# Optimization experiments

Hardware: AMD Instinct MI355X
Metric: run time of the kernel (lower is better)

## Reference

```python
import jax, jax.numpy as jnp
import numpy as np

D_MODEL = 512
NUM_HEADS = 8
D_HEAD = 64
B, T = 8, 1024


def sinusoidal_pos(start, end, d, dtype=jnp.float32):
    # positions start .. end-1, standard sinusoidal encoding, shape (1, end-start, d)
    pos = jnp.arange(start, end, dtype=jnp.float32)[:, None]              # (L,1)
    inv_freq = jnp.exp(-jnp.log(10000.0) * jnp.arange(0, d, 2, dtype=jnp.float32) / d)
    ang = pos * inv_freq[None, :]                                          # (L,d/2)
    pe = jnp.stack([jnp.sin(ang), jnp.cos(ang)], axis=-1).reshape(pos.shape[0], d)
    return pe[None].astype(dtype)                                          # (1,L,d)


def _relative_shift(x):
    # x: (B,H,T,L) -> Transformer-XL shift trick
    b, h, t, l = x.shape
    x = jnp.pad(x, ((0, 0), (0, 0), (0, 0), (1, 0)))                       # (B,H,T,L+1)
    x = x.reshape(b, h, l + 1, t)[:, :, 1:, :].reshape(b, h, t, l)
    return x


def setup_inputs() -> dict:
    key = jax.random.key(0)
    ks = jax.random.split(key, 8)
    hd = NUM_HEADS * D_HEAD
    s_in = 1.0 / np.sqrt(D_MODEL)
    s_out = 1.0 / np.sqrt(hd)
    return {
        "xs": jax.random.normal(ks[0], (B, T, D_MODEL), jnp.float32),
        "mask": jnp.ones((B, T, T), jnp.int32),
        "Wq": jax.random.normal(ks[1], (D_MODEL, hd), jnp.float32) * s_in,
        "Wk": jax.random.normal(ks[2], (D_MODEL, hd), jnp.float32) * s_in,
        "Wv": jax.random.normal(ks[3], (D_MODEL, hd), jnp.float32) * s_in,
        "Wpos": jax.random.normal(ks[4], (D_MODEL, hd), jnp.float32) * s_in,
        "Wout": jax.random.normal(ks[5], (hd, D_MODEL), jnp.float32) * s_out,
        "u_bias": jax.random.normal(ks[6], (NUM_HEADS, D_HEAD), jnp.float32) * 0.02,
        "v_bias": jax.random.normal(ks[7], (NUM_HEADS, D_HEAD), jnp.float32) * 0.02,
    }


def reference(xs, mask, Wq, Wk, Wv, Wpos, Wout, u_bias, v_bias):
    b, t, _ = xs.shape
    scale = 1.0 / np.sqrt(D_HEAD)

    def split_heads(y):  # (B,T,H*dh) -> (B,H,T,dh)
        return y.reshape(b, t, NUM_HEADS, D_HEAD).transpose(0, 2, 1, 3)

    q = split_heads(xs @ Wq)
    k = split_heads(xs @ Wk)
    v = split_heads(xs @ Wv)

    # positions -(T-1) .. T-1, length 2T-1
    pos_enc = sinusoidal_pos(-(t - 1), t, D_MODEL, xs.dtype)               # (1,L,D)
    p = (pos_enc[0] @ Wpos).reshape(-1, NUM_HEADS, D_HEAD).transpose(1, 0, 2)  # (H,L,dh)

    q_u = q + u_bias[None, :, None, :]
    q_v = q + v_bias[None, :, None, :]

    matrix_ac = jnp.einsum("bhtd,bhsd->bhts", q_u, k)                      # (B,H,T,T)
    matrix_bd = jnp.einsum("bhtd,hld->bhtl", q_v, p)                       # (B,H,T,2T-1)
    matrix_bd = _relative_shift(matrix_bd)[:, :, :, :t]                    # (B,H,T,T)

    scores = (matrix_ac + matrix_bd) * scale

    m = (mask[:, None, :, :] == 0)                                          # (B,1,T,T)
    scores = jnp.where(m, -jnp.inf, scores)
    attn = jax.nn.softmax(scores, axis=-1)
    attn = jnp.where(m, 0.0, attn)
    # dropout is identity in eval mode

    z = jnp.einsum("bhts,bhsd->bthd", attn, v).reshape(b, t, NUM_HEADS * D_HEAD)
    return z @ Wout
```

## Files before the change

### kernel.cpp

```cpp
#include <hip/hip_runtime.h>
#include <hip/hip_bf16.h>


typedef unsigned short u16;
typedef unsigned long long u64;
typedef __attribute__((ext_vector_type(8))) short bf16x8;
typedef __attribute__((ext_vector_type(8))) unsigned short ushort8v;
typedef __attribute__((ext_vector_type(4))) float floatx4;

__device__ __forceinline__ float b2f(u16 u) {
    union { unsigned int i; float f; } x; x.i = ((unsigned int)u) << 16; return x.f;
}
__device__ __forceinline__ u16 f2b(float f) {
    __hip_bfloat16 h = __float2bfloat16(f);
    return *reinterpret_cast<u16*>(&h);
}

#define MFMA16(a, b, c) __builtin_amdgcn_mfma_f32_16x16x32_bf16(a, b, c, 0, 0, 0)

__global__ __launch_bounds__(256) void prep_kernel(
    const float* __restrict__ X, u16* __restrict__ Xb,
    const float* __restrict__ W0, const float* __restrict__ W1,
    const float* __restrict__ W2, const float* __restrict__ W3,
    const float* __restrict__ W4, u16* __restrict__ WT,
    const int* __restrict__ mask, u64* __restrict__ Mp,
    u16* __restrict__ Peb)
{
    const int bi = blockIdx.x;
    const int tid = threadIdx.x;
    if (bi < 2048) {
        size_t i = ((size_t)bi * 256 + tid) * 8;
        float4 a = *(const float4*)&X[i];
        float4 b = *(const float4*)&X[i + 4];
        ushort8v s;
        s[0] = f2b(a.x); s[1] = f2b(a.y); s[2] = f2b(a.z); s[3] = f2b(a.w);
        s[4] = f2b(b.x); s[5] = f2b(b.y); s[6] = f2b(b.z); s[7] = f2b(b.w);
        *(ushort8v*)&Xb[i] = s;
    } else if (bi < 2368) {
        __shared__ float t[64][68];
        const int li = bi - 2048;
        const int m = li >> 6;
        const float* src = (m == 0) ? W0 : (m == 1) ? W1 : (m == 2) ? W2
                         : (m == 3) ? W3 : W4;
        u16* dst = WT + (size_t)m * 262144;
        const int sub = li & 63;
        const int k0 = ((sub >> 3) & 7) * 64, n0 = (sub & 7) * 64;
        const int r = tid >> 4, c = tid & 15;
#pragma unroll
        for (int rr = 0; rr < 64; rr += 16) {
            float4 v = *(const float4*)&src[(size_t)(k0 + r + rr) * 512 + n0 + 4 * c];
            t[r + rr][4 * c + 0] = v.x;
            t[r + rr][4 * c + 1] = v.y;
            t[r + rr][4 * c + 2] = v.z;
            t[r + rr][4 * c + 3] = v.w;
        }
        __syncthreads();
        const int nrow = tid >> 2, kc = (tid & 3) * 16;
        ushort8v s0, s1;
#pragma unroll
        for (int e = 0; e < 8; ++e) {
            s0[e] = f2b(t[kc + e][nrow]);
            s1[e] = f2b(t[kc + 8 + e][nrow]);
        }
        *(ushort8v*)&dst[(size_t)(n0 + nrow) * 512 + k0 + kc] = s0;
        *(ushort8v*)&dst[(size_t)(n0 + nrow) * 512 + k0 + kc + 8] = s1;
    } else if (bi < 4416) {
        const int lane = tid & 63, w = tid >> 6;
        const int row = (bi - 2368) * 4 + w;
#pragma unroll
        for (int j = 0; j < 16; ++j) {
            int v = mask[(size_t)row * 1024 + j * 64 + lane];
            u64 bits = __ballot(v != 0);
            if (lane == j) Mp[(size_t)row * 16 + j] = bits;
        }
    } else {
        const int lane = tid & 63, w = tid >> 6;
        const int l = (bi - 4416) * 4 + w;
        const int lc = (l > 2046) ? 2046 : l;
        const float pos = (float)(lc - 1023);
        ushort8v s;
#pragma unroll
        for (int e = 0; e < 8; ++e) {
            int k = (lane << 3) + e;
            int i = k >> 1;
            float invf = expf(-0.035977892f * (float)i);
            float ang = pos * invf;
            float v = (k & 1) ? cosf(ang) : sinf(ang);
            s[e] = f2b(v);
        }
        *(ushort8v*)&Peb[(size_t)l * 512 + (lane << 3)] = s;
    }
}

__global__ __launch_bounds__(256, 2) void qkv_mfma(
    const u16* __restrict__ Xb, const u16* __restrict__ WqT,
    const u16* __restrict__ WkT, const u16* __restrict__ WvT,
    const u16* __restrict__ Peb, const u16* __restrict__ WposT,
    u16* __restrict__ Qb, u16* __restrict__ Kb, u16* __restrict__ Vtg,
    u16* __restrict__ Pg)
{
    __shared__ u16 Xl[128 * 40];
    __shared__ u16 Wl[128 * 40];
    const int tid = threadIdx.x;
    const int lane = tid & 63, w = tid >> 6;
    const int quad = lane >> 4, ln = lane & 15;
    const int wm = w & 1, wn = w >> 1;

    const int yy = blockIdx.y;
    int sel, m0, n0;
    const u16 *Ap, *Bp;
    if (yy < 12) {
        sel = yy >> 2; n0 = (yy & 3) * 128; m0 = blockIdx.x * 128;
        Ap = Xb; Bp = (sel == 0) ? WqT : (sel == 1) ? WkT : WvT;
    } else {
        sel = 3; m0 = (blockIdx.x >> 2) * 128; n0 = (blockIdx.x & 3) * 128;
        Ap = Peb; Bp = WposT;
    }
    const int b = (m0 >> 10) & 7, tbase = m0 & 1023;

    const int sr = tid >> 2, sg = tid & 3;

    floatx4 acc[4][4];
#pragma unroll
    for (int i = 0; i < 4; ++i)
#pragma unroll
        for (int j = 0; j < 4; ++j) acc[i][j] = (floatx4){0.f, 0.f, 0.f, 0.f};

    ushort8v xq[2], wq2[2];
#pragma unroll
    for (int it = 0; it < 2; ++it) {
        int r = sr + it * 64;
        xq[it]  = *(const ushort8v*)&Ap[(size_t)(m0 + r) * 512 + sg * 8];
        wq2[it] = *(const ushort8v*)&Bp[(size_t)(n0 + r) * 512 + sg * 8];
    }

    for (int kc = 0; kc < 512; kc += 32) {
        __syncthreads();
#pragma unroll
        for (int it = 0; it < 2; ++it) {
            int r = sr + it * 64;
            *(ushort8v*)&Xl[r * 40 + sg * 8] = xq[it];
            *(ushort8v*)&Wl[r * 40 + sg * 8] = wq2[it];
        }
        __syncthreads();
        if (kc + 32 < 512) {
#pragma unroll
            for (int it = 0; it < 2; ++it) {
                int r = sr + it * 64;
                xq[it]  = *(const ushort8v*)&Ap[(size_t)(m0 + r) * 512 + kc + 32 + sg * 8];
                wq2[it] = *(const ushort8v*)&Bp[(size_t)(n0 + r) * 512 + kc + 32 + sg * 8];
            }
        }
        bf16x8 am[4], an[4];
#pragma unroll
        for (int i = 0; i < 4; ++i)
            am[i] = *(bf16x8*)&Xl[(wm * 64 + i * 16 + ln) * 40 + quad * 8];
#pragma unroll
        for (int j = 0; j < 4; ++j)
            an[j] = *(bf16x8*)&Wl[(wn * 64 + j * 16 + ln) * 40 + quad * 8];
        if (sel != 2) {
#pragma unroll
            for (int i = 0; i < 4; ++i)
#pragma unroll
                for (int j = 0; j < 4; ++j)
                    acc[i][j] = MFMA16(an[j], am[i], acc[i][j]);
        } else {
#pragma unroll
            for (int i = 0; i < 4; ++i)
#pragma unroll
                for (int j = 0; j < 4; ++j)
                    acc[i][j] = MFMA16(am[i], an[j], acc[i][j]);
        }
    }
    if (sel < 2) {
        u16* dst = (sel == 0) ? Qb : Kb;
#pragma unroll
        for (int i = 0; i < 4; ++i) {
            int t = tbase + wm * 64 + i * 16 + ln;
#pragma unroll
            for (int j = 0; j < 4; ++j) {
                int n = n0 + wn * 64 + j * 16 + quad * 4;
                int h = n >> 6, d = n & 63;
                ushort4 s;
                s.x = f2b(acc[i][j][0]); s.y = f2b(acc[i][j][1]);
                s.z = f2b(acc[i][j][2]); s.w = f2b(acc[i][j][3]);
                *(ushort4*)&dst[(((size_t)b * 8 + h) * 1024 + t) * 64 + d] = s;
            }
        }
    } else if (sel == 2) {
#pragma unroll
        for (int i = 0; i < 4; ++i) {
            int t4 = tbase + wm * 64 + i * 16 + quad * 4;
#pragma unroll
            for (int j = 0; j < 4; ++j) {
                int n = n0 + wn * 64 + j * 16 + ln;
                int h = n >> 6, d = n & 63;
                ushort4 s;
                s.x = f2b(acc[i][j][0]); s.y = f2b(acc[i][j][1]);
                s.z = f2b(acc[i][j][2]); s.w = f2b(acc[i][j][3]);
                *(ushort4*)&Vtg[(((size_t)b * 8 + h) * 64 + d) * 1024 + t4] = s;
            }
        }
    } else {
#pragma unroll
        for (int i = 0; i < 4; ++i) {
            int l = m0 + wm * 64 + i * 16 + ln;
#pragma unroll
            for (int j = 0; j < 4; ++j) {
                int n = n0 + wn * 64 + j * 16 + quad * 4;
                int h = n >> 6, d = n & 63;
                ushort4 s;
                s.x = f2b(acc[i][j][0]); s.y = f2b(acc[i][j][1]);
                s.z = f2b(acc[i][j][2]); s.w = f2b(acc[i][j][3]);
                *(ushort4*)&Pg[(((size_t)h << 11) + l) * 64 + d] = s;
            }
        }
    }
}

__device__ __forceinline__ bf16x8 addbias(bf16x8 q, const float* __restrict__ bias) {
    float4 a = *(const float4*)&bias[0];
    float4 b = *(const float4*)&bias[4];
    bf16x8 r;
    r[0] = (short)f2b(b2f((u16)q[0]) + a.x);
    r[1] = (short)f2b(b2f((u16)q[1]) + a.y);
    r[2] = (short)f2b(b2f((u16)q[2]) + a.z);
    r[3] = (short)f2b(b2f((u16)q[3]) + a.w);
    r[4] = (short)f2b(b2f((u16)q[4]) + b.x);
    r[5] = (short)f2b(b2f((u16)q[5]) + b.y);
    r[6] = (short)f2b(b2f((u16)q[6]) + b.z);
    r[7] = (short)f2b(b2f((u16)q[7]) + b.w);
    return r;
}

__global__ __launch_bounds__(256, 2) void attn_mfma(
    const u16* __restrict__ Qb,
    const u16* __restrict__ Kb, const u16* __restrict__ Vtg,
    const u16* __restrict__ P, const u64* __restrict__ Mp,
    const float* __restrict__ ub, const float* __restrict__ vb,
    u16* __restrict__ Z)
{
    __shared__ u16 Pb[2][192 * 64];
    __shared__ __align__(16) char WaveBuf[4][16 * 80 * 4];

    const int tid  = threadIdx.x;
    const int lane = tid & 63;
    const int w    = tid >> 6;
    const int quad = lane >> 4;
    const int ln   = lane & 15;

    const int bid = blockIdx.x;
    const int xg  = bid & 7;
    const int idx = bid >> 3;
    const int bh_i = xg * 8 + (idx >> 3);
    const int t0 = (idx & 7) << 7;
    const int h  = bh_i & 7;
    const int b  = bh_i >> 3;
    const size_t bh  = (size_t)bh_i * 1024;
    const size_t bhd = (size_t)bh_i * 64;
    size_t mprow[2];
    mprow[0] = ((size_t)b * 1024 + t0 + 16 * w + ln) * 16;
    mprow[1] = ((size_t)b * 1024 + t0 + 64 + 16 * w + ln) * 16;

    bf16x8 qu0[2], qu1[2], qv0[2], qv1[2];
#pragma unroll
    for (int c = 0; c < 2; ++c) {
        const size_t qoff = (bh + t0 + 64 * c + 16 * w + ln) * 64;
        bf16x8 q0 = *(const bf16x8*)&Qb[qoff + quad * 8];
        bf16x8 q1 = *(const bf16x8*)&Qb[qoff + 32 + quad * 8];
        qu0[c] = addbias(q0, &ub[h * 64 + quad * 8]);
        qu1[c] = addbias(q1, &ub[h * 64 + 32 + quad * 8]);
        qv0[c] = addbias(q0, &vb[h * 64 + quad * 8]);
        qv1[c] = addbias(q1, &vb[h * 64 + 32 + quad * 8]);
    }

    floatx4 O[2][4];
#pragma unroll
    for (int c = 0; c < 2; ++c)
#pragma unroll
        for (int dt = 0; dt < 4; ++dt) O[c][dt] = (floatx4){0.f, 0.f, 0.f, 0.f};
    float m_run[2] = {-3.0e38f, -3.0e38f}, l_run[2] = {0.f, 0.f};

    float* gw = (float*)&WaveBuf[w][0];
    u16*  pw  = (u16*)&WaveBuf[w][0];

    const int str = tid >> 3, stg = tid & 7;
    ushort8v pq[6];

    {
        const int lb0 = 896 - t0;
#pragma unroll
        for (int it = 0; it < 6; ++it) {
            int r = str + it * 32;
            pq[it] = *(const ushort8v*)&P[((((size_t)h << 11) + (size_t)(lb0 + r)) << 6) + stg * 8];
        }
    }

    for (int i = 0; i < 16; ++i) {
        const int s0 = i << 6;
        u16* pb = &Pb[i & 1][0];

#pragma unroll
        for (int it = 0; it < 6; ++it) {
            int r = str + it * 32;
            *(ushort8v*)&pb[r * 64 + ((stg ^ (r & 7)) << 3)] = pq[it];
        }
        __syncthreads();

        if (i < 15) {
            const int lb0 = 896 - t0 + s0 + 64;
#pragma unroll
            for (int it = 0; it < 6; ++it) {
                int r = str + it * 32;
                pq[it] = *(const ushort8v*)&P[((((size_t)h << 11) + (size_t)(lb0 + r)) << 6) + stg * 8];
            }
        }

        bf16x8 kf[4][2], vf[4][2];
#pragma unroll
        for (int st = 0; st < 4; ++st) {
            const u16* kp = &Kb[(bh + s0 + st * 16 + ln) * 64 + quad * 8];
            kf[st][0] = *(const bf16x8*)(kp);
            kf[st][1] = *(const bf16x8*)(kp + 32);
        }
#pragma unroll
        for (int dt = 0; dt < 4; ++dt) {
            const u16* vp = &Vtg[(bhd + dt * 16 + ln) * 1024 + s0 + quad * 8];
            vf[dt][0] = *(const bf16x8*)(vp);
            vf[dt][1] = *(const bf16x8*)(vp + 32);
        }

#pragma unroll
        for (int c = 0; c < 2; ++c) {
            const u64 bits = Mp[mprow[c] + i];
            const int rb0 = 112 - 64 * c - 16 * w;
#pragma unroll
            for (int jt = 0; jt < 5; ++jt) {
                int rb = rb0 + jt * 16 + ln;
                bf16x8 a0 = *(bf16x8*)&pb[rb * 64 + ((quad ^ (rb & 7)) << 3)];
                bf16x8 a1 = *(bf16x8*)&pb[rb * 64 + (((4 + quad) ^ (rb & 7)) << 3)];
                floatx4 g = {0.f, 0.f, 0.f, 0.f};
                g = MFMA16(a0, qv0[c], g);
                g = MFMA16(a1, qv1[c], g);
                *(floatx4*)&gw[ln * 80 + jt * 16 + quad * 4] = g;
            }
            floatx4 cac[4];
#pragma unroll
            for (int st = 0; st < 4; ++st) {
                floatx4 cc = {0.f, 0.f, 0.f, 0.f};
                cc = MFMA16(kf[st][0], qu0[c], cc);
                cc = MFMA16(kf[st][1], qu1[c], cc);
                cac[st] = cc;
            }
            float sc[4][4];
            float cmax = -3.0e38f;
#pragma unroll
            for (int st = 0; st < 4; ++st) {
                int j0 = st * 16 + quad * 4 + 15 - ln;
#pragma unroll
                for (int r = 0; r < 4; ++r) {
                    float v = (cac[st][r] + gw[ln * 80 + j0 + r]) * 0.125f;
                    int ss = st * 16 + quad * 4 + r;
                    v = ((bits >> ss) & 1ull) ? v : -1.0e30f;
                    sc[st][r] = v;
                    cmax = fmaxf(cmax, v);
                }
            }
            cmax = fmaxf(cmax, __shfl_xor(cmax, 16));
            cmax = fmaxf(cmax, __shfl_xor(cmax, 32));
            float m_new = fmaxf(m_run[c], cmax);
            float alpha = __expf(m_run[c] - m_new);
            float psum = 0.f;
#pragma unroll
            for (int st = 0; st < 4; ++st) {
                float p0 = __expf(sc[st][0] - m_new);
                float p1 = __expf(sc[st][1] - m_new);
                float p2 = __expf(sc[st][2] - m_new);
                float p3 = __expf(sc[st][3] - m_new);
                psum += (p0 + p1) + (p2 + p3);
                ushort4 pk;
                pk.x = f2b(p0); pk.y = f2b(p1); pk.z = f2b(p2); pk.w = f2b(p3);
                *(ushort4*)&pw[ln * 72 + st * 16 + quad * 4] = pk;
            }
            psum += __shfl_xor(psum, 16);
            psum += __shfl_xor(psum, 32);
            l_run[c] = l_run[c] * alpha + psum;
            m_run[c] = m_new;
            float a0s = __shfl(alpha, quad * 4 + 0);
            float a1s = __shfl(alpha, quad * 4 + 1);
            float a2s = __shfl(alpha, quad * 4 + 2);
            float a3s = __shfl(alpha, quad * 4 + 3);
#pragma unroll
            for (int dt = 0; dt < 4; ++dt) {
                O[c][dt][0] *= a0s; O[c][dt][1] *= a1s;
                O[c][dt][2] *= a2s; O[c][dt][3] *= a3s;
            }
            bf16x8 pa0 = *(bf16x8*)&pw[ln * 72 + quad * 8];
            bf16x8 pa1 = *(bf16x8*)&pw[ln * 72 + 32 + quad * 8];
#pragma unroll
            for (int dt = 0; dt < 4; ++dt) {
                O[c][dt] = MFMA16(pa0, vf[dt][0], O[c][dt]);
                O[c][dt] = MFMA16(pa1, vf[dt][1], O[c][dt]);
            }
        }
    }
#pragma unroll
    for (int c = 0; c < 2; ++c) {
        float li[4];
#pragma unroll
        for (int r = 0; r < 4; ++r) li[r] = 1.0f / __shfl(l_run[c], quad * 4 + r);
#pragma unroll
        for (int r = 0; r < 4; ++r) {
            size_t zo = ((size_t)b * 1024 + t0 + 64 * c + 16 * w + quad * 4 + r) * 512
                      + h * 64 + ln;
            Z[zo + 0]  = f2b(O[c][0][r] * li[r]);
            Z[zo + 16] = f2b(O[c][1][r] * li[r]);
            Z[zo + 32] = f2b(O[c][2][r] * li[r]);
            Z[zo + 48] = f2b(O[c][3][r] * li[r]);
        }
    }
}

__global__ __launch_bounds__(256, 2) void out_mfma(
    const u16* __restrict__ Zb, const u16* __restrict__ WoT,
    float* __restrict__ out)
{
    __shared__ u16 Xl[128 * 40];
    __shared__ u16 Wl[128 * 40];
    const int tid = threadIdx.x;
    const int lane = tid & 63, w = tid >> 6;
    const int quad = lane >> 4, ln = lane & 15;
    const int wm = w & 1, wn = w >> 1;
    const int m0 = blockIdx.x * 128;
    const int n0 = blockIdx.y * 128;
    const int sr = tid >> 2, sg = tid & 3;

    floatx4 acc[4][4];
#pragma unroll
    for (int i = 0; i < 4; ++i)
#pragma unroll
        for (int j = 0; j < 4; ++j) acc[i][j] = (floatx4){0.f, 0.f, 0.f, 0.f};

    ushort8v xq[2], wq2[2];
#pragma unroll
    for (int it = 0; it < 2; ++it) {
        int r = sr + it * 64;
        xq[it]  = *(const ushort8v*)&Zb[(size_t)(m0 + r) * 512 + sg * 8];
        wq2[it] = *(const ushort8v*)&WoT[(size_t)(n0 + r) * 512 + sg * 8];
    }

    for (int kc = 0; kc < 512; kc += 32) {
        __syncthreads();
#pragma unroll
        for (int it = 0; it < 2; ++it) {
            int r = sr + it * 64;
            *(ushort8v*)&Xl[r * 40 + sg * 8] = xq[it];
            *(ushort8v*)&Wl[r * 40 + sg * 8] = wq2[it];
        }
        __syncthreads();
        if (kc + 32 < 512) {
#pragma unroll
            for (int it = 0; it < 2; ++it) {
                int r = sr + it * 64;
                xq[it]  = *(const ushort8v*)&Zb[(size_t)(m0 + r) * 512 + kc + 32 + sg * 8];
                wq2[it] = *(const ushort8v*)&WoT[(size_t)(n0 + r) * 512 + kc + 32 + sg * 8];
            }
        }
        bf16x8 am[4], an[4];
#pragma unroll
        for (int i = 0; i < 4; ++i)
            am[i] = *(bf16x8*)&Xl[(wm * 64 + i * 16 + ln) * 40 + quad * 8];
#pragma unroll
        for (int j = 0; j < 4; ++j)
            an[j] = *(bf16x8*)&Wl[(wn * 64 + j * 16 + ln) * 40 + quad * 8];
#pragma unroll
        for (int i = 0; i < 4; ++i)
#pragma unroll
            for (int j = 0; j < 4; ++j)
                acc[i][j] = MFMA16(an[j], am[i], acc[i][j]);
    }
#pragma unroll
    for (int i = 0; i < 4; ++i) {
        int m = m0 + wm * 64 + i * 16 + ln;
#pragma unroll
        for (int j = 0; j < 4; ++j) {
            int n = n0 + wn * 64 + j * 16 + quad * 4;
            float4 s;
            s.x = acc[i][j][0]; s.y = acc[i][j][1];
            s.z = acc[i][j][2]; s.w = acc[i][j][3];
            *(float4*)&out[(size_t)m * 512 + n] = s;
        }
    }
}

extern "C" void kernel_launch(void* const* d_in, const int* in_sizes, int n_in,
                              void* d_out, int out_size, void* d_ws, size_t ws_size,
                              hipStream_t stream) {
    const float* xs   = (const float*)d_in[0];
    const int*   mask = (const int*)d_in[1];
    const float* Wq   = (const float*)d_in[2];
    const float* Wk   = (const float*)d_in[3];
    const float* Wv   = (const float*)d_in[4];
    const float* Wpos = (const float*)d_in[5];
    const float* Wout = (const float*)d_in[6];
    const float* ub   = (const float*)d_in[7];
    const float* vb   = (const float*)d_in[8];
    float* out = (float*)d_out;

    u16* Qb  = (u16*)d_ws;
    u16* Kb  = Qb + 4194304;
    u16* Vtg = Kb + 4194304;
    u16* Pg  = Vtg + 4194304;
    u16* XZ  = Pg + 1048576;
    u16* WT  = XZ + 4194304;
    u16* WqT = WT;
    u16* WkT = WT + 262144;
    u16* WvT = WT + 524288;
    u16* WoT = WT + 786432;
    u16* WposT = WT + 1048576;
    u16* Peb = WT + 1310720;
    u64* Mp  = (u64*)(Peb + 1048576);

    prep_kernel<<<4928, 256, 0, stream>>>(xs, XZ, Wq, Wk, Wv, Wout, Wpos, WT,
                                          mask, Mp, Peb);
    qkv_mfma<<<dim3(64, 13), 256, 0, stream>>>(XZ, WqT, WkT, WvT, Peb, WposT,
                                               Qb, Kb, Vtg, Pg);
    attn_mfma<<<512, 256, 0, stream>>>(Qb, Kb, Vtg, Pg, Mp, ub, vb, XZ);
    out_mfma<<<dim3(64, 4), 256, 0, stream>>>(XZ, WoT, out);
}
```

Measured before the change: 243.1 us.

## Double-buffer K fragments and mask bits across attention chunks, pad wave buffer

Prefetches the next chunk's K fragments and mask bits into alternating register sets, using a manually unrolled two-chunk macro so the loads overlap the current chunk's MFMA and softmax work. The per-wave scratch stride also changes from 80 to 84 floats, which is meant to reduce LDS bank conflicts on the gw reads and writes. The cost is higher register pressure from the duplicated K fragment sets, which could lower occupancy under launch_bounds(256,2) or cause spills.

```diff
diff --git a/kernel.cpp b/kernel.cpp
--- a/kernel.cpp
+++ b/kernel.cpp
@@ -241,7 +241,7 @@
     u16* __restrict__ Z)
 {
     __shared__ u16 Pb[2][192 * 64];
-    __shared__ __align__(16) char WaveBuf[4][16 * 80 * 4];
+    __shared__ __align__(16) char WaveBuf[4][16 * 84 * 4];
 
     const int tid  = threadIdx.x;
     const int lane = tid & 63;
@@ -286,6 +286,8 @@
 
     const int str = tid >> 3, stg = tid & 7;
     ushort8v pq[6];
+    bf16x8 kfA[4][2], kfB[4][2];
+    u64 bitsA[2], bitsB[2];
 
     {
         const int lb0 = 896 - t0;
@@ -294,116 +296,131 @@
             int r = str + it * 32;
             pq[it] = *(const ushort8v*)&P[((((size_t)h << 11) + (size_t)(lb0 + r)) << 6) + stg * 8];
         }
-    }
-
-    for (int i = 0; i < 16; ++i) {
-        const int s0 = i << 6;
-        u16* pb = &Pb[i & 1][0];
-
-#pragma unroll
-        for (int it = 0; it < 6; ++it) {
-            int r = str + it * 32;
-            *(ushort8v*)&pb[r * 64 + ((stg ^ (r & 7)) << 3)] = pq[it];
-        }
-        __syncthreads();
-
-        if (i < 15) {
-            const int lb0 = 896 - t0 + s0 + 64;
-#pragma unroll
-            for (int it = 0; it < 6; ++it) {
-                int r = str + it * 32;
-                pq[it] = *(const ushort8v*)&P[((((size_t)h << 11) + (size_t)(lb0 + r)) << 6) + stg * 8];
-            }
-        }
-
-        bf16x8 kf[4][2], vf[4][2];
 #pragma unroll
         for (int st = 0; st < 4; ++st) {
-            const u16* kp = &Kb[(bh + s0 + st * 16 + ln) * 64 + quad * 8];
-            kf[st][0] = *(const bf16x8*)(kp);
-            kf[st][1] = *(const bf16x8*)(kp + 32);
-        }
-#pragma unroll
-        for (int dt = 0; dt < 4; ++dt) {
-            const u16* vp = &Vtg[(bhd + dt * 16 + ln) * 1024 + s0 + quad * 8];
-            vf[dt][0] = *(const bf16x8*)(vp);
-            vf[dt][1] = *(const bf16x8*)(vp + 32);
-        }
-
-#pragma unroll
-        for (int c = 0; c < 2; ++c) {
-            const u64 bits = Mp[mprow[c] + i];
-            const int rb0 = 112 - 64 * c - 16 * w;
-#pragma unroll
-            for (int jt = 0; jt < 5; ++jt) {
-                int rb = rb0 + jt * 16 + ln;
-                bf16x8 a0 = *(bf16x8*)&pb[rb * 64 + ((quad ^ (rb & 7)) << 3)];
-                bf16x8 a1 = *(bf16x8*)&pb[rb * 64 + (((4 + quad) ^ (rb & 7)) << 3)];
-                floatx4 g = {0.f, 0.f, 0.f, 0.f};
-                g = MFMA16(a0, qv0[c], g);
-                g = MFMA16(a1, qv1[c], g);
-                *(floatx4*)&gw[ln * 80 + jt * 16 + quad * 4] = g;
-            }
-            floatx4 cac[4];
-#pragma unroll
-            for (int st = 0; st < 4; ++st) {
-                floatx4 cc = {0.f, 0.f, 0.f, 0.f};
-                cc = MFMA16(kf[st][0], qu0[c], cc);
-                cc = MFMA16(kf[st][1], qu1[c], cc);
-                cac[st] = cc;
-            }
-            float sc[4][4];
-            float cmax = -3.0e38f;
-#pragma unroll
-            for (int st = 0; st < 4; ++st) {
-                int j0 = st * 16 + quad * 4 + 15 - ln;
-#pragma unroll
-                for (int r = 0; r < 4; ++r) {
-                    float v = (cac[st][r] + gw[ln * 80 + j0 + r]) * 0.125f;
-                    int ss = st * 16 + quad * 4 + r;
-                    v = ((bits >> ss) & 1ull) ? v : -1.0e30f;
-                    sc[st][r] = v;
-                    cmax = fmaxf(cmax, v);
-                }
-            }
-            cmax = fmaxf(cmax, __shfl_xor(cmax, 16));
-            cmax = fmaxf(cmax, __shfl_xor(cmax, 32));
-            float m_new = fmaxf(m_run[c], cmax);
-            float alpha = __expf(m_run[c] - m_new);
-            float psum = 0.f;
-#pragma unroll
-            for (int st = 0; st < 4; ++st) {
-                float p0 = __expf(sc[st][0] - m_new);
-                float p1 = __expf(sc[st][1] - m_new);
-                float p2 = __expf(sc[st][2] - m_new);
-                float p3 = __expf(sc[st][3] - m_new);
-                psum += (p0 + p1) + (p2 + p3);
-                ushort4 pk;
-                pk.x = f2b(p0); pk.y = f2b(p1); pk.z = f2b(p2); pk.w = f2b(p3);
-                *(ushort4*)&pw[ln * 72 + st * 16 + quad * 4] = pk;
-            }
-            psum += __shfl_xor(psum, 16);
-            psum += __shfl_xor(psum, 32);
-            l_run[c] = l_run[c] * alpha + psum;
-            m_run[c] = m_new;
-            float a0s = __shfl(alpha, quad * 4 + 0);
-            float a1s = __shfl(alpha, quad * 4 + 1);
-            float a2s = __shfl(alpha, quad * 4 + 2);
-            float a3s = __shfl(alpha, quad * 4 + 3);
-#pragma unroll
-            for (int dt = 0; dt < 4; ++dt) {
-                O[c][dt][0] *= a0s; O[c][dt][1] *= a1s;
-                O[c][dt][2] *= a2s; O[c][dt][3] *= a3s;
-            }
-            bf16x8 pa0 = *(bf16x8*)&pw[ln * 72 + quad * 8];
-            bf16x8 pa1 = *(bf16x8*)&pw[ln * 72 + 32 + quad * 8];
-#pragma unroll
-            for (int dt = 0; dt < 4; ++dt) {
-                O[c][dt] = MFMA16(pa0, vf[dt][0], O[c][dt]);
-                O[c][dt] = MFMA16(pa1, vf[dt][1], O[c][dt]);
-            }
-        }
-    }
+            const u16* kp = &Kb[(bh + st * 16 + ln) * 64 + quad * 8];
+            kfA[st][0] = *(const bf16x8*)(kp);
+            kfA[st][1] = *(const bf16x8*)(kp + 32);
+        }
+        bitsA[0] = Mp[mprow[0]];
+        bitsA[1] = Mp[mprow[1]];
+    }
+
+#define ATTN_CHUNK(IDX, KFC, KFN, BTC, BTN)                                       \
+    {                                                                             \
+        const int i_ = (IDX);                                                     \
+        const int s0 = i_ << 6;                                                   \
+        u16* pb = &Pb[i_ & 1][0];                                                 \
+        _Pragma("unroll")                                                         \
+        for (int it = 0; it < 6; ++it) {                                          \
+            int r = str + it * 32;                                                \
+            *(ushort8v*)&pb[r * 64 + ((stg ^ (r & 7)) << 3)] = pq[it];            \
+        }                                                                         \
+        __syncthreads();                                                          \
+        bf16x8 vf[4][2];                                                          \
+        _Pragma("unroll")                                                         \
+        for (int dt = 0; dt < 4; ++dt) {                                          \
+            const u16* vp = &Vtg[(bhd + dt * 16 + ln) * 1024 + s0 + quad * 8];    \
+            vf[dt][0] = *(const bf16x8*)(vp);                                     \
+            vf[dt][1] = *(const bf16x8*)(vp + 32);                                \
+        }                                                                         \
+        if (i_ < 15) {                                                            \
+            _Pragma("unroll")                                                     \
+            for (int st = 0; st < 4; ++st) {                                      \
+                const u16* kp = &Kb[(bh + s0 + 64 + st * 16 + ln) * 64 + quad * 8]; \
+                KFN[st][0] = *(const bf16x8*)(kp);                                \
+                KFN[st][1] = *(const bf16x8*)(kp + 32);                           \
+            }                                                                     \
+            BTN[0] = Mp[mprow[0] + i_ + 1];                                       \
+            BTN[1] = Mp[mprow[1] + i_ + 1];                                       \
+            const int lb0 = 896 - t0 + s0 + 64;                                   \
+            _Pragma("unroll")                                                     \
+            for (int it = 0; it < 6; ++it) {                                      \
+                int r = str + it * 32;                                            \
+                pq[it] = *(const ushort8v*)&P[((((size_t)h << 11) + (size_t)(lb0 + r)) << 6) + stg * 8]; \
+            }                                                                     \
+        }                                                                         \
+        _Pragma("unroll")                                                         \
+        for (int c = 0; c < 2; ++c) {                                             \
+            const u64 bits = BTC[c];                                              \
+            const int rb0 = 112 - 64 * c - 16 * w;                                \
+            _Pragma("unroll")                                                     \
+            for (int jt = 0; jt < 5; ++jt) {                                      \
+                int rb = rb0 + jt * 16 + ln;                                      \
+                bf16x8 a0 = *(bf16x8*)&pb[rb * 64 + ((quad ^ (rb & 7)) << 3)];    \
+                bf16x8 a1 = *(bf16x8*)&pb[rb * 64 + (((4 + quad) ^ (rb & 7)) << 3)]; \
+                floatx4 g = {0.f, 0.f, 0.f, 0.f};                                 \
+                g = MFMA16(a0, qv0[c], g);                                        \
+                g = MFMA16(a1, qv1[c], g);                                        \
+                *(floatx4*)&gw[ln * 84 + jt * 16 + quad * 4] = g;                 \
+            }                                                                     \
+            floatx4 cac[4];                                                       \
+            _Pragma("unroll")                                                     \
+            for (int st = 0; st < 4; ++st) {                                      \
+                floatx4 cc = {0.f, 0.f, 0.f, 0.f};                                \
+                cc = MFMA16(KFC[st][0], qu0[c], cc);                              \
+                cc = MFMA16(KFC[st][1], qu1[c], cc);                              \
+                cac[st] = cc;                                                     \
+            }                                                                     \
+            float sc[4][4];                                                       \
+            float cmax = -3.0e38f;                                                \
+            _Pragma("unroll")                                                     \
+            for (int st = 0; st < 4; ++st) {                                      \
+                int j0 = st * 16 + quad * 4 + 15 - ln;                            \
+                _Pragma("unroll")                                                 \
+                for (int r = 0; r < 4; ++r) {                                     \
+                    float v = (cac[st][r] + gw[ln * 84 + j0 + r]) * 0.125f;       \
+                    int ss = st * 16 + quad * 4 + r;                              \
+                    v = ((bits >> ss) & 1ull) ? v : -1.0e30f;                     \
+                    sc[st][r] = v;                                                \
+                    cmax = fmaxf(cmax, v);                                        \
+                }                                                                 \
+            }                                                                     \
+            cmax = fmaxf(cmax, __shfl_xor(cmax, 16));                             \
+            cmax = fmaxf(cmax, __shfl_xor(cmax, 32));                             \
+            float m_new = fmaxf(m_run[c], cmax);                                  \
+            float alpha = __expf(m_run[c] - m_new);                               \
+            float psum = 0.f;                                                     \
+            _Pragma("unroll")                                                     \
+            for (int st = 0; st < 4; ++st) {                                      \
+                float p0 = __expf(sc[st][0] - m_new);                             \
+                float p1 = __expf(sc[st][1] - m_new);                             \
+                float p2 = __expf(sc[st][2] - m_new);                             \
+                float p3 = __expf(sc[st][3] - m_new);                             \
+                psum += (p0 + p1) + (p2 + p3);                                    \
+                ushort4 pk;                                                       \
+                pk.x = f2b(p0); pk.y = f2b(p1); pk.z = f2b(p2); pk.w = f2b(p3);   \
+                *(ushort4*)&pw[ln * 72 + st * 16 + quad * 4] = pk;                \
+            }                                                                     \
+            psum += __shfl_xor(psum, 16);                                         \
+            psum += __shfl_xor(psum, 32);                                         \
+            l_run[c] = l_run[c] * alpha + psum;                                   \
+            m_run[c] = m_new;                                                     \
+            float a0s = __shfl(alpha, quad * 4 + 0);                              \
+            float a1s = __shfl(alpha, quad * 4 + 1);                              \
+            float a2s = __shfl(alpha, quad * 4 + 2);                              \
+            float a3s = __shfl(alpha, quad * 4 + 3);                              \
+            _Pragma("unroll")                                                     \
+            for (int dt = 0; dt < 4; ++dt) {                                      \
+                O[c][dt][0] *= a0s; O[c][dt][1] *= a1s;                           \
+                O[c][dt][2] *= a2s; O[c][dt][3] *= a3s;                           \
+            }                                                                     \
+            bf16x8 pa0 = *(bf16x8*)&pw[ln * 72 + quad * 8];                       \
+            bf16x8 pa1 = *(bf16x8*)&pw[ln * 72 + 32 + quad * 8];                  \
+            _Pragma("unroll")                                                     \
+            for (int dt = 0; dt < 4; ++dt) {                                      \
+                O[c][dt] = MFMA16(pa0, vf[dt][0], O[c][dt]);                      \
+                O[c][dt] = MFMA16(pa1, vf[dt][1], O[c][dt]);                      \
+            }                                                                     \
+        }                                                                         \
+    }
+
+    for (int ii = 0; ii < 16; ii += 2) {
+        ATTN_CHUNK(ii,     kfA, kfB, bitsA, bitsB)
+        ATTN_CHUNK(ii + 1, kfB, kfA, bitsB, bitsA)
+    }
+#undef ATTN_CHUNK
+
 #pragma unroll
     for (int c = 0; c < 2; ++c) {
         float li[4];
```

Result: slower. 288.6 us (+18.7%).
